# Kernel tuning notes

Measured on AMD Instinct MI355X. Metric: run time of the kernel, lower is better.

The kernel has to match this reference:

```python
import math
import jax, jax.numpy as jnp
import numpy as np

B, T, C = 2, 768, 64
N_HEAD = 64
HEAD_DIM = C // N_HEAD  # = 1 (forced by the Kronecker-lift shape constraint)


def _alibi_slopes(n_heads):
    def pow2_slopes(n):
        start = 2 ** (-2 ** (-(math.log2(n) - 3)))
        return [start * (start ** i) for i in range(n)]
    if math.log2(n_heads).is_integer():
        s = pow2_slopes(n_heads)
    else:
        closest = 2 ** math.floor(math.log2(n_heads))
        s = pow2_slopes(closest)
        s.extend(pow2_slopes(2 * closest)[0::2][: n_heads - closest])
    return np.asarray(s, dtype=np.float32)


def _kron_block_apply(z, tmp):
    """Apply M.T where M = block_diag_h(kron(eye(hd), tmp[h])). z:(B,T,C), tmp:(H,hd,hd).
    Per head-block, for z reshaped (a,d) over (hd,hd): out[a,c] = sum_d tmp[h,c,d] * z[a,d]."""
    Bz, Tz, Cz = z.shape
    H, hd, _ = tmp.shape
    zr = z.reshape(Bz, Tz, H, hd, hd)
    return jnp.einsum('bthad,hcd->bthac', zr, tmp).reshape(Bz, Tz, Cz)


def setup_inputs() -> dict:
    key = jax.random.key(0)
    kx, kw, kv, kp = jax.random.split(key, 4)
    x = jax.random.normal(kx, (B, T, C), dtype=jnp.float32)
    W_attn = jax.random.normal(kw, (2 * C, C), dtype=jnp.float32) * 0.02
    v_tmp = jax.random.normal(kv, (N_HEAD, HEAD_DIM, HEAD_DIM), dtype=jnp.float32)
    proj_tmp = jax.random.normal(kp, (N_HEAD, HEAD_DIM, HEAD_DIM), dtype=jnp.float32)
    return {"x": x, "W_attn": W_attn, "v_tmp": v_tmp, "proj_tmp": proj_tmp}


def reference(x, W_attn, v_tmp, proj_tmp):
    Bx, Tx, Cx = x.shape
    H = v_tmp.shape[0]
    head_dim = Cx // H
    # q, k projection (use_v=True -> c_attn maps C -> 2C, no bias)
    qk = x @ W_attn.T
    q, k = jnp.split(qk, 2, axis=-1)
    # Kronecker-lifted V transform (block-diagonal structure applied directly)
    v = _kron_block_apply(x, v_tmp)
    # (B,T,H,d) -> (B,H,T,d)
    q = q.reshape(Bx, Tx, H, head_dim).transpose(0, 2, 1, 3)
    k = k.reshape(Bx, Tx, H, head_dim).transpose(0, 2, 1, 3)
    v = v.reshape(Bx, Tx, H, head_dim).transpose(0, 2, 1, 3)
    scale = 1.0 / math.sqrt(head_dim)
    scores = jnp.einsum('bhid,bhjd->bhij', q, k) * scale
    # ALiBi bias: positions clamped at 0 (NOTE: source has no causal -inf mask)
    pos = jnp.minimum(jnp.arange(Tx)[None, :] - jnp.arange(Tx)[:, None], 0).astype(x.dtype)
    slopes = jnp.asarray(_alibi_slopes(H), dtype=x.dtype)
    scores = scores + slopes[None, :, None, None] * pos[None, None, :, :]
    w = jax.nn.softmax(scores, axis=-1)
    y = jnp.einsum('bhij,bhjd->bhid', w, v)
    y = y.transpose(0, 2, 1, 3).reshape(Bx, Tx, Cx)
    # Kronecker-lifted output projection
    y = _kron_block_apply(y, proj_tmp)
    return y
```

## Files before the change

kernel.cpp:

```cpp
#include <hip/hip_runtime.h>
#include <stdint.h>

constexpr int Tc = 768;
constexpr int Hc = 64;
constexpr int Bc = 2;
constexpr int NT = 12;
constexpr float LOG2E = 1.44269504088896f;
constexpr float LN2   = 0.69314718056f;
constexpr size_t SLAB = (size_t)Bc * Hc * Tc;

typedef float v2f __attribute__((ext_vector_type(2)));
typedef float v4f __attribute__((ext_vector_type(4)));

__global__ __launch_bounds__(64) void proj_mom_kernel(
    const float* __restrict__ x, const float* __restrict__ W,
    const float* __restrict__ vtmp, const float* __restrict__ ptmp,
    float* __restrict__ qs, float* __restrict__ ks, float* __restrict__ vs,
    float* __restrict__ MOM)
{
    const int lane = threadIdx.x & 63;
    const int bx   = blockIdx.x;
    const int b    = bx / NT;
    const int B    = bx - b * NT;
    const int t    = B * 64 + lane;
    const int g    = bx * 64 + lane;
    const int h    = blockIdx.y;
    const int bh   = b * Hc + h;

    const v4f* xp = (const v4f*)(x + (size_t)g * 64);
    const float* __restrict__ wq = W + h * 64;
    const float* __restrict__ wk = W + (64 + h) * 64;
    float aq = 0.f, ak = 0.f;
#pragma unroll
    for (int c = 0; c < 16; ++c) {
        v4f u = xp[c];
        aq = fmaf(u.x, wq[4*c],   aq);  ak = fmaf(u.x, wk[4*c],   ak);
        aq = fmaf(u.y, wq[4*c+1], aq);  ak = fmaf(u.y, wk[4*c+1], ak);
        aq = fmaf(u.z, wq[4*c+2], aq);  ak = fmaf(u.z, wk[4*c+2], ak);
        aq = fmaf(u.w, wq[4*c+3], aq);  ak = fmaf(u.w, wk[4*c+3], ak);
    }
    const float vv = x[(size_t)g * 64 + h] * vtmp[h] * ptmp[h];
    const size_t o = (size_t)bh * Tc + t;
    qs[o] = aq * LOG2E;
    ks[o] = ak;
    vs[o] = vv;

    const float slope2 = exp2f(-0.125f * (float)(h + 1)) * LOG2E;
    const float lf = exp2f(slope2 * (float)(lane - 63));

    float km[8];
    km[0] = 1.f;
#pragma unroll
    for (int m = 1; m < 8; ++m) km[m] = km[m - 1] * ak;

    float r[32];
#pragma unroll
    for (int m = 0; m < 8; ++m) {
        const float kl2 = km[m] * lf;
        r[m]      = km[m];
        r[8 + m]  = km[m] * vv;
        r[16 + m] = kl2;
        r[24 + m] = kl2 * vv;
    }
#define DPP_PASS(CTRL)                                                        \
    _Pragma("unroll")                                                         \
    for (int ii = 0; ii < 32; ++ii)                                           \
        r[ii] += __int_as_float(__builtin_amdgcn_update_dpp(                  \
            0, __float_as_int(r[ii]), CTRL, 0xf, 0xf, true));
    DPP_PASS(0x111)
    DPP_PASS(0x112)
    DPP_PASS(0x114)
    DPP_PASS(0x118)
    DPP_PASS(0x142)
    DPP_PASS(0x143)
#undef DPP_PASS

    if (lane == 63) {
        float* mp = MOM + ((size_t)bh * NT + B) * 32;
#pragma unroll
        for (int m = 0; m < 8; ++m) {
            v4f s4 = { r[4*m], r[4*m+1], r[4*m+2], r[4*m+3] };
            *(v4f*)(mp + 4 * m) = s4;
        }
    }
}

__global__ __launch_bounds__(256, 6) void attn_kernel(
    const float* __restrict__ qs, const float* __restrict__ ks,
    const float* __restrict__ vs, const float* __restrict__ MOM,
    float* __restrict__ out)
{
    const int tid  = threadIdx.x;
    const int lane = tid & 63;
    const int w    = __builtin_amdgcn_readfirstlane(tid >> 6);
    const int rt   = blockIdx.x;
    const int h    = blockIdx.y;
    const int b    = blockIdx.z;
    const int bh   = b * Hc + h;

    __shared__ float momL[NT * 32];
    __shared__ float kd[64], vd[64];
    __shared__ float comb[32];
    __shared__ float psum[4][64], pacc[4][64];

    {
        const float* __restrict__ mbp = MOM + (size_t)bh * (NT * 32);
        if (tid < 128) {
            momL[tid]       = mbp[tid];
            momL[tid + 128] = mbp[tid + 128];
            momL[tid + 256] = mbp[tid + 256];
        } else if (tid < 192) {
            kd[tid - 128] = ks[(size_t)bh * Tc + rt * 64 + (tid - 128)];
        } else {
            vd[tid - 192] = vs[(size_t)bh * Tc + rt * 64 + (tid - 192)];
        }
    }
    const float slope2 = exp2f(-0.125f * (float)(h + 1)) * LOG2E;
    __syncthreads();

    if (tid < 32) {
        const int grp = tid >> 4;
        const int m16 = tid & 15;
        float acc = 0.f;
        if (grp == 0) {
            for (int B = rt + 1; B < NT; ++B)
                acc += momL[B * 32 + m16];
        } else {
            for (int B = 0; B < rt; ++B)
                acc = fmaf(exp2f(slope2 * (float)(64 * (B - rt) + 63)),
                           momL[B * 32 + 16 + m16], acc);
        }
        comb[tid] = acc;
    }
    __syncthreads();

    const int i = rt * 64 + lane;
    const float q2 = qs[(size_t)bh * Tc + i];
    const float fi2 = slope2 * (float)i;

    const float z  = q2 * LN2;
    const float p1 = z;
    const float p2 = z * p1 * 0.5f;
    const float p3 = z * p2 * (1.f / 3.f);
    const float p4 = z * p3 * 0.25f;
    const float p5 = z * p4 * 0.2f;
    const float p6 = z * p5 * (1.f / 6.f);
    const float p7 = z * p6 * (1.f / 7.f);

    float S = 0.f, A = 0.f;
    if (w == 0) {
        float sf = comb[0];
        sf = fmaf(p1, comb[1], sf); sf = fmaf(p2, comb[2], sf);
        sf = fmaf(p3, comb[3], sf); sf = fmaf(p4, comb[4], sf);
        sf = fmaf(p5, comb[5], sf); sf = fmaf(p6, comb[6], sf);
        sf = fmaf(p7, comb[7], sf);
        float af = comb[8];
        af = fmaf(p1, comb[9],  af); af = fmaf(p2, comb[10], af);
        af = fmaf(p3, comb[11], af); af = fmaf(p4, comb[12], af);
        af = fmaf(p5, comb[13], af); af = fmaf(p6, comb[14], af);
        af = fmaf(p7, comb[15], af);
        float sp = comb[16];
        sp = fmaf(p1, comb[17], sp); sp = fmaf(p2, comb[18], sp);
        sp = fmaf(p3, comb[19], sp); sp = fmaf(p4, comb[20], sp);
        sp = fmaf(p5, comb[21], sp); sp = fmaf(p6, comb[22], sp);
        sp = fmaf(p7, comb[23], sp);
        float ap = comb[24];
        ap = fmaf(p1, comb[25], ap); ap = fmaf(p2, comb[26], ap);
        ap = fmaf(p3, comb[27], ap); ap = fmaf(p4, comb[28], ap);
        ap = fmaf(p5, comb[29], ap); ap = fmaf(p6, comb[30], ap);
        ap = fmaf(p7, comb[31], ap);
        const float f = __builtin_amdgcn_exp2f(-slope2 * (float)lane);
        S = fmaf(f, sp, sf);
        A = fmaf(f, ap, af);
    }

    v2f cu2[8];
#pragma unroll
    for (int u = 0; u < 8; ++u) {
        cu2[u].x = slope2 * (float)(2 * u);
        cu2[u].y = slope2 * (float)(2 * u + 1);
    }
    const float mb = slope2 * (float)(rt * 64 + 16 * w) - fi2;
    const v2f mb2 = {mb, mb};
    const v2f q2v = {q2, q2};
    v2f sum2 = {0.f, 0.f}, acc2 = {0.f, 0.f};
    const v2f* __restrict__ k2p = (const v2f*)kd;
    const v2f* __restrict__ v2p = (const v2f*)vd;
#pragma unroll
    for (int u = 0; u < 8; ++u) {
        v2f k2 = k2p[8 * w + u];
        v2f v2 = v2p[8 * w + u];
        v2f t2 = mb2 + cu2[u];
        v2f bias;
        bias.x = fminf(t2.x, 0.f);
        bias.y = fminf(t2.y, 0.f);
        v2f sc = q2v * k2 + bias;
        v2f e;
        e.x = __builtin_amdgcn_exp2f(sc.x);
        e.y = __builtin_amdgcn_exp2f(sc.y);
        sum2 += e;
        acc2 = e * v2 + acc2;
    }
    S += sum2.x + sum2.y;
    A += acc2.x + acc2.y;

    psum[w][lane] = S;
    pacc[w][lane] = A;
    __syncthreads();

    if (tid < 64) {
        float s = psum[0][lane] + psum[1][lane] + psum[2][lane] + psum[3][lane];
        float a = pacc[0][lane] + pacc[1][lane] + pacc[2][lane] + pacc[3][lane];
        out[((size_t)(b * Tc + rt * 64 + lane)) * 64 + h] =
            a * __builtin_amdgcn_rcpf(s);
    }
}

extern "C" void kernel_launch(void* const* d_in, const int* in_sizes, int n_in,
                              void* d_out, int out_size, void* d_ws, size_t ws_size,
                              hipStream_t stream) {
    const float* x    = (const float*)d_in[0];
    const float* W    = (const float*)d_in[1];
    const float* vtmp = (const float*)d_in[2];
    const float* ptmp = (const float*)d_in[3];
    float* out = (float*)d_out;

    float* qsl = (float*)d_ws;
    float* ksl = qsl + SLAB;
    float* vsl = ksl + SLAB;
    float* mom = vsl + SLAB;

    proj_mom_kernel<<<dim3(24, Hc), 64, 0, stream>>>(
        x, W, vtmp, ptmp, qsl, ksl, vsl, mom);
    attn_kernel<<<dim3(NT, Hc, Bc), 256, 0, stream>>>(
        qsl, ksl, vsl, mom, out);
}
```

Measured before the change: 66.78 us.

## Fuse projection/moment kernel into attention kernel with per-block recompute

Merges the projection and moment kernel and the attention kernel into one launch. Each block handles half the sequence for one (b,h) and recomputes q/k/v projections and moments for all 12 tiles into shared memory, removing the workspace round trip and the second launch. Each wave now owns one 64-row tile and loops over its 64 diagonal keys directly, replacing the 4-way split with its cross-wave reduction. In exchange, projection work is done twice per (b,h), and only 256 blocks of 384 threads are launched, which lowers parallelism.

```diff
diff --git a/kernel.cpp b/kernel.cpp
--- a/kernel.cpp
+++ b/kernel.cpp
@@ -7,122 +7,98 @@
 constexpr int NT = 12;
 constexpr float LOG2E = 1.44269504088896f;
 constexpr float LN2   = 0.69314718056f;
-constexpr size_t SLAB = (size_t)Bc * Hc * Tc;
 
 typedef float v2f __attribute__((ext_vector_type(2)));
 typedef float v4f __attribute__((ext_vector_type(4)));
 
-__global__ __launch_bounds__(64) void proj_mom_kernel(
+__global__ __launch_bounds__(384) void fused_attn_kernel(
     const float* __restrict__ x, const float* __restrict__ W,
     const float* __restrict__ vtmp, const float* __restrict__ ptmp,
-    float* __restrict__ qs, float* __restrict__ ks, float* __restrict__ vs,
-    float* __restrict__ MOM)
+    float* __restrict__ out)
 {
-    const int lane = threadIdx.x & 63;
-    const int bx   = blockIdx.x;
-    const int b    = bx / NT;
-    const int B    = bx - b * NT;
-    const int t    = B * 64 + lane;
-    const int g    = bx * 64 + lane;
+    const int tid  = threadIdx.x;
+    const int lane = tid & 63;
+    const int w    = __builtin_amdgcn_readfirstlane(tid >> 6);
+    const int half = blockIdx.x;
     const int h    = blockIdx.y;
-    const int bh   = b * Hc + h;
+    const int b    = blockIdx.z;
 
-    const v4f* xp = (const v4f*)(x + (size_t)g * 64);
+    __shared__ float momL[NT * 32];
+    __shared__ float kdL[384], vdL[384], qL[384];
+    __shared__ float combL[6 * 32];
+
+    const float slope2 = exp2f(-0.125f * (float)(h + 1)) * LOG2E;
+    const float vscale = vtmp[h] * ptmp[h];
+    const float lf = exp2f(slope2 * (float)(lane - 63));
     const float* __restrict__ wq = W + h * 64;
     const float* __restrict__ wk = W + (64 + h) * 64;
-    float aq = 0.f, ak = 0.f;
+
+    for (int it = 0; it < 2; ++it) {
+        const int Bj = it * 6 + w;
+        const int p  = Bj * 64 + lane;
+        const v4f* xp = (const v4f*)(x + ((size_t)(b * Tc + p)) * 64);
+        float aq = 0.f, ak = 0.f;
 #pragma unroll
-    for (int c = 0; c < 16; ++c) {
-        v4f u = xp[c];
-        aq = fmaf(u.x, wq[4*c],   aq);  ak = fmaf(u.x, wk[4*c],   ak);
-        aq = fmaf(u.y, wq[4*c+1], aq);  ak = fmaf(u.y, wk[4*c+1], ak);
-        aq = fmaf(u.z, wq[4*c+2], aq);  ak = fmaf(u.z, wk[4*c+2], ak);
-        aq = fmaf(u.w, wq[4*c+3], aq);  ak = fmaf(u.w, wk[4*c+3], ak);
-    }
-    const float vv = x[(size_t)g * 64 + h] * vtmp[h] * ptmp[h];
-    const size_t o = (size_t)bh * Tc + t;
-    qs[o] = aq * LOG2E;
-    ks[o] = ak;
-    vs[o] = vv;
+        for (int c = 0; c < 16; ++c) {
+            v4f u = xp[c];
+            aq = fmaf(u.x, wq[4*c],   aq);  ak = fmaf(u.x, wk[4*c],   ak);
+            aq = fmaf(u.y, wq[4*c+1], aq);  ak = fmaf(u.y, wk[4*c+1], ak);
+            aq = fmaf(u.z, wq[4*c+2], aq);  ak = fmaf(u.z, wk[4*c+2], ak);
+            aq = fmaf(u.w, wq[4*c+3], aq);  ak = fmaf(u.w, wk[4*c+3], ak);
+        }
+        const float vv = x[((size_t)(b * Tc + p)) * 64 + h] * vscale;
+        if (it == half) {
+            const int loc = w * 64 + lane;
+            qL[loc]  = aq * LOG2E;
+            kdL[loc] = ak;
+            vdL[loc] = vv;
+        }
 
-    const float slope2 = exp2f(-0.125f * (float)(h + 1)) * LOG2E;
-    const float lf = exp2f(slope2 * (float)(lane - 63));
+        float km[8];
+        km[0] = 1.f;
+#pragma unroll
+        for (int m = 1; m < 8; ++m) km[m] = km[m - 1] * ak;
 
-    float km[8];
-    km[0] = 1.f;
+        float r[32];
 #pragma unroll
-    for (int m = 1; m < 8; ++m) km[m] = km[m - 1] * ak;
-
-    float r[32];
-#pragma unroll
-    for (int m = 0; m < 8; ++m) {
-        const float kl2 = km[m] * lf;
-        r[m]      = km[m];
-        r[8 + m]  = km[m] * vv;
-        r[16 + m] = kl2;
-        r[24 + m] = kl2 * vv;
-    }
+        for (int m = 0; m < 8; ++m) {
+            const float kl2 = km[m] * lf;
+            r[m]      = km[m];
+            r[8 + m]  = km[m] * vv;
+            r[16 + m] = kl2;
+            r[24 + m] = kl2 * vv;
+        }
 #define DPP_PASS(CTRL)                                                        \
     _Pragma("unroll")                                                         \
     for (int ii = 0; ii < 32; ++ii)                                           \
         r[ii] += __int_as_float(__builtin_amdgcn_update_dpp(                  \
             0, __float_as_int(r[ii]), CTRL, 0xf, 0xf, true));
-    DPP_PASS(0x111)
-    DPP_PASS(0x112)
-    DPP_PASS(0x114)
-    DPP_PASS(0x118)
-    DPP_PASS(0x142)
-    DPP_PASS(0x143)
+        DPP_PASS(0x111)
+        DPP_PASS(0x112)
+        DPP_PASS(0x114)
+        DPP_PASS(0x118)
+        DPP_PASS(0x142)
+        DPP_PASS(0x143)
 #undef DPP_PASS
 
-    if (lane == 63) {
-        float* mp = MOM + ((size_t)bh * NT + B) * 32;
+        if (lane == 63) {
+            float* mp = momL + Bj * 32;
 #pragma unroll
-        for (int m = 0; m < 8; ++m) {
-            v4f s4 = { r[4*m], r[4*m+1], r[4*m+2], r[4*m+3] };
-            *(v4f*)(mp + 4 * m) = s4;
+            for (int m = 0; m < 8; ++m) {
+                v4f s4 = { r[4*m], r[4*m+1], r[4*m+2], r[4*m+3] };
+                *(v4f*)(mp + 4 * m) = s4;
+            }
         }
     }
-}
-
-__global__ __launch_bounds__(256, 6) void attn_kernel(
-    const float* __restrict__ qs, const float* __restrict__ ks,
-    const float* __restrict__ vs, const float* __restrict__ MOM,
-    float* __restrict__ out)
-{
-    const int tid  = threadIdx.x;
-    const int lane = tid & 63;
-    const int w    = __builtin_amdgcn_readfirstlane(tid >> 6);
-    const int rt   = blockIdx.x;
-    const int h    = blockIdx.y;
-    const int b    = blockIdx.z;
-    const int bh   = b * Hc + h;
-
-    __shared__ float momL[NT * 32];
-    __shared__ float kd[64], vd[64];
-    __shared__ float comb[32];
-    __shared__ float psum[4][64], pacc[4][64];
-
-    {
-        const float* __restrict__ mbp = MOM + (size_t)bh * (NT * 32);
-        if (tid < 128) {
-            momL[tid]       = mbp[tid];
-            momL[tid + 128] = mbp[tid + 128];
-            momL[tid + 256] = mbp[tid + 256];
-        } else if (tid < 192) {
-            kd[tid - 128] = ks[(size_t)bh * Tc + rt * 64 + (tid - 128)];
-        } else {
-            vd[tid - 192] = vs[(size_t)bh * Tc + rt * 64 + (tid - 192)];
-        }
-    }
-    const float slope2 = exp2f(-0.125f * (float)(h + 1)) * LOG2E;
     __syncthreads();
 
-    if (tid < 32) {
-        const int grp = tid >> 4;
-        const int m16 = tid & 15;
+    if (tid < 192) {
+        const int lt  = tid >> 5;
+        const int idx = tid & 31;
+        const int rt  = half * 6 + lt;
+        const int m16 = idx & 15;
         float acc = 0.f;
-        if (grp == 0) {
+        if (idx < 16) {
             for (int B = rt + 1; B < NT; ++B)
                 acc += momL[B * 32 + m16];
         } else {
@@ -130,13 +106,13 @@
                 acc = fmaf(exp2f(slope2 * (float)(64 * (B - rt) + 63)),
                            momL[B * 32 + 16 + m16], acc);
         }
-        comb[tid] = acc;
+        combL[lt * 32 + idx] = acc;
     }
     __syncthreads();
 
-    const int i = rt * 64 + lane;
-    const float q2 = qs[(size_t)bh * Tc + i];
-    const float fi2 = slope2 * (float)i;
+    const int rt = half * 6 + w;
+    const int i  = rt * 64 + lane;
+    const float q2 = qL[w * 64 + lane];
 
     const float z  = q2 * LN2;
     const float p1 = z;
@@ -147,73 +123,48 @@
     const float p6 = z * p5 * (1.f / 6.f);
     const float p7 = z * p6 * (1.f / 7.f);
 
-    float S = 0.f, A = 0.f;
-    if (w == 0) {
-        float sf = comb[0];
-        sf = fmaf(p1, comb[1], sf); sf = fmaf(p2, comb[2], sf);
-        sf = fmaf(p3, comb[3], sf); sf = fmaf(p4, comb[4], sf);
-        sf = fmaf(p5, comb[5], sf); sf = fmaf(p6, comb[6], sf);
-        sf = fmaf(p7, comb[7], sf);
-        float af = comb[8];
-        af = fmaf(p1, comb[9],  af); af = fmaf(p2, comb[10], af);
-        af = fmaf(p3, comb[11], af); af = fmaf(p4, comb[12], af);
-        af = fmaf(p5, comb[13], af); af = fmaf(p6, comb[14], af);
-        af = fmaf(p7, comb[15], af);
-        float sp = comb[16];
-        sp = fmaf(p1, comb[17], sp); sp = fmaf(p2, comb[18], sp);
-        sp = fmaf(p3, comb[19], sp); sp = fmaf(p4, comb[20], sp);
-        sp = fmaf(p5, comb[21], sp); sp = fmaf(p6, comb[22], sp);
-        sp = fmaf(p7, comb[23], sp);
-        float ap = comb[24];
-        ap = fmaf(p1, comb[25], ap); ap = fmaf(p2, comb[26], ap);
-        ap = fmaf(p3, comb[27], ap); ap = fmaf(p4, comb[28], ap);
-        ap = fmaf(p5, comb[29], ap); ap = fmaf(p6, comb[30], ap);
-        ap = fmaf(p7, comb[31], ap);
-        const float f = __builtin_amdgcn_exp2f(-slope2 * (float)lane);
-        S = fmaf(f, sp, sf);
-        A = fmaf(f, ap, af);
+    const float* __restrict__ cb = combL + w * 32;
+    float sf = cb[0];
+    sf = fmaf(p1, cb[1], sf); sf = fmaf(p2, cb[2], sf);
+    sf = fmaf(p3, cb[3], sf); sf = fmaf(p4, cb[4], sf);
+    sf = fmaf(p5, cb[5], sf); sf = fmaf(p6, cb[6], sf);
+    sf = fmaf(p7, cb[7], sf);
+    float af = cb[8];
+    af = fmaf(p1, cb[9],  af); af = fmaf(p2, cb[10], af);
+    af = fmaf(p3, cb[11], af); af = fmaf(p4, cb[12], af);
+    af = fmaf(p5, cb[13], af); af = fmaf(p6, cb[14], af);
+    af = fmaf(p7, cb[15], af);
+    float sp = cb[16];
+    sp = fmaf(p1, cb[17], sp); sp = fmaf(p2, cb[18], sp);
+    sp = fmaf(p3, cb[19], sp); sp = fmaf(p4, cb[20], sp);
+    sp = fmaf(p5, cb[21], sp); sp = fmaf(p6, cb[22], sp);
+    sp = fmaf(p7, cb[23], sp);
+    float ap = cb[24];
+    ap = fmaf(p1, cb[25], ap); ap = fmaf(p2, cb[26], ap);
+    ap = fmaf(p3, cb[27], ap); ap = fmaf(p4, cb[28], ap);
+    ap = fmaf(p5, cb[29], ap); ap = fmaf(p6, cb[30], ap);
+    ap = fmaf(p7, cb[31], ap);
+    const float f = __builtin_amdgcn_exp2f(-slope2 * (float)lane);
+    float S = fmaf(f, sp, sf);
+    float A = fmaf(f, ap, af);
+
+    const float negl = -slope2 * (float)lane;
+    const v2f* __restrict__ k2p = (const v2f*)kdL + w * 32;
+    const v2f* __restrict__ v2p = (const v2f*)vdL + w * 32;
+#pragma unroll
+    for (int u = 0; u < 32; ++u) {
+        v2f k2 = k2p[u];
+        v2f v2 = v2p[u];
+        const float t0 = fminf(fmaf(slope2, (float)(2 * u),     negl), 0.f);
+        const float t1 = fminf(fmaf(slope2, (float)(2 * u + 1), negl), 0.f);
+        const float e0 = __builtin_amdgcn_exp2f(fmaf(q2, k2.x, t0));
+        const float e1 = __builtin_amdgcn_exp2f(fmaf(q2, k2.y, t1));
+        S += e0 + e1;
+        A = fmaf(e0, v2.x, A);
+        A = fmaf(e1, v2.y, A);
     }
 
-    v2f cu2[8];
-#pragma unroll
-    for (int u = 0; u < 8; ++u) {
-        cu2[u].x = slope2 * (float)(2 * u);
-        cu2[u].y = slope2 * (float)(2 * u + 1);
-    }
-    const float mb = slope2 * (float)(rt * 64 + 16 * w) - fi2;
-    const v2f mb2 = {mb, mb};
-    const v2f q2v = {q2, q2};
-    v2f sum2 = {0.f, 0.f}, acc2 = {0.f, 0.f};
-    const v2f* __restrict__ k2p = (const v2f*)kd;
-    const v2f* __restrict__ v2p = (const v2f*)vd;
-#pragma unroll
-    for (int u = 0; u < 8; ++u) {
-        v2f k2 = k2p[8 * w + u];
-        v2f v2 = v2p[8 * w + u];
-        v2f t2 = mb2 + cu2[u];
-        v2f bias;
-        bias.x = fminf(t2.x, 0.f);
-        bias.y = fminf(t2.y, 0.f);
-        v2f sc = q2v * k2 + bias;
-        v2f e;
-        e.x = __builtin_amdgcn_exp2f(sc.x);
-        e.y = __builtin_amdgcn_exp2f(sc.y);
-        sum2 += e;
-        acc2 = e * v2 + acc2;
-    }
-    S += sum2.x + sum2.y;
-    A += acc2.x + acc2.y;
-
-    psum[w][lane] = S;
-    pacc[w][lane] = A;
-    __syncthreads();
-
-    if (tid < 64) {
-        float s = psum[0][lane] + psum[1][lane] + psum[2][lane] + psum[3][lane];
-        float a = pacc[0][lane] + pacc[1][lane] + pacc[2][lane] + pacc[3][lane];
-        out[((size_t)(b * Tc + rt * 64 + lane)) * 64 + h] =
-            a * __builtin_amdgcn_rcpf(s);
-    }
+    out[((size_t)(b * Tc + i)) * 64 + h] = A * __builtin_amdgcn_rcpf(S);
 }
 
 extern "C" void kernel_launch(void* const* d_in, const int* in_sizes, int n_in,
@@ -224,14 +175,8 @@
     const float* vtmp = (const float*)d_in[2];
     const float* ptmp = (const float*)d_in[3];
     float* out = (float*)d_out;
+    (void)d_ws; (void)ws_size;
 
-    float* qsl = (float*)d_ws;
-    float* ksl = qsl + SLAB;
-    float* vsl = ksl + SLAB;
-    float* mom = vsl + SLAB;
-
-    proj_mom_kernel<<<dim3(24, Hc), 64, 0, stream>>>(
-        x, W, vtmp, ptmp, qsl, ksl, vsl, mom);
-    attn_kernel<<<dim3(NT, Hc, Bc), 256, 0, stream>>>(
-        qsl, ksl, vsl, mom, out);
+    fused_attn_kernel<<<dim3(2, Hc, Bc), 384, 0, stream>>>(
+        x, W, vtmp, ptmp, out);
 }
```

New measurement: 69.19 us. 3.6% more time.
